# Optimization experiments

Measured on AMD Instinct MI355X. Metric: run time of the kernel, lower is better.

Reference implementation:

```python
import jax, jax.numpy as jnp
import numpy as np

N_OBJ = 4096
IN_DIM = 1024
OUT_DIM = 1024
H = OUT_DIM // 2  # per-direction hidden, BidirectionalTreeLSTM uses out_dim//2
L = 2             # num_layer


def _build_tree(n):
    # balanced binary heap tree: node i has children 2i+1, 2i+2
    left = np.array([2 * i + 1 if 2 * i + 1 < n else -1 for i in range(n)], np.int32)
    right = np.array([2 * i + 2 if 2 * i + 2 < n else -1 for i in range(n)], np.int32)
    parent = np.full(n, -1, np.int32)
    for i in range(n):
        if left[i] >= 0:
            parent[left[i]] = i
        if right[i] >= 0:
            parent[right[i]] = i
    post, stack = [], [(0, False)]
    while stack:
        node, seen = stack.pop()
        if node < 0:
            continue
        if seen:
            post.append(node)
        else:
            stack.append((node, True))
            stack.append((int(right[node]), False))
            stack.append((int(left[node]), False))
    pre, stack = [], [0]
    while stack:
        node = stack.pop()
        if node < 0:
            continue
        pre.append(node)
        stack.append(int(right[node]))
        stack.append(int(left[node]))
    pad = lambda a: np.where(a < 0, n, a).astype(np.int32)  # slot n = zeros (no child/parent)
    return (np.array(post, np.int32), np.array(pre, np.int32),
            pad(left), pad(right), pad(parent))


def setup_inputs() -> dict:
    key = jax.random.key(0)
    ks = jax.random.split(key, 8)
    post, pre, left, right, parent = _build_tree(N_OBJ)

    def w(k, shape, fan_in):
        return jax.random.normal(k, shape, jnp.float32) * np.float32(1.0 / np.sqrt(fan_in))

    # bias init per the torch module: forget-gate blocks get constants, rest zero
    fw_bl = np.zeros((L, 6 * H), np.float32); fw_bl[:, 2 * H:4 * H] = 0.5
    fw_br = fw_bl.copy()
    bw_bh = np.zeros((L, 5 * H), np.float32); bw_bh[:, 2 * H:3 * H] = 1.0

    return {
        "features": jax.random.normal(ks[0], (N_OBJ, IN_DIM), jnp.float32),
        "fw_Wp": w(ks[1], (L, H, IN_DIM), IN_DIM),
        "fw_bp": jnp.zeros((L, H), jnp.float32),
        "fw_Wx": w(ks[2], (L, 6 * H, IN_DIM), IN_DIM),
        "fw_bx": jnp.zeros((L, 6 * H), jnp.float32),
        "fw_Wl": w(ks[3], (L, 6 * H, H), H),
        "fw_bl": jnp.asarray(fw_bl),
        "fw_Wr": w(ks[4], (L, 6 * H, H), H),
        "fw_br": jnp.asarray(fw_br),
        "bw_Wp": w(ks[5], (L, H, IN_DIM), IN_DIM),
        "bw_bp": jnp.zeros((L, H), jnp.float32),
        "bw_Wx": w(ks[6], (L, 5 * H, IN_DIM), IN_DIM),
        "bw_bx": jnp.zeros((L, 5 * H), jnp.float32),
        "bw_Wh": w(ks[7], (L, 5 * H, H), H),
        "bw_bh": jnp.asarray(bw_bh),
        "post_order": jnp.asarray(post),
        "pre_order": jnp.asarray(pre),
        "left_child": jnp.asarray(left),
        "right_child": jnp.asarray(right),
        "parent": jnp.asarray(parent),
    }


def _tree_leaves_to_root(feats, Wp, bp, Wx, bx, Wl, bl, Wr, br,
                         post_order, left_child, right_child):
    n = feats.shape[0]
    h = bp.shape[0]
    px = feats @ Wp.T + bp   # [n, h]   -- self path
    x2 = feats @ Wx.T + bx   # [n, 6h]  -- gate input, batched once

    def step(carry, idx):
        cbuf, hbuf = carry   # [n+1, h]; row n is permanent zero slot for missing children
        lc = left_child[idx]
        rc = right_child[idx]
        g = x2[idx] + hbuf[lc] @ Wl.T + bl + hbuf[rc] @ Wr.T + br
        i, o, fl, fr, u, r = jnp.split(g, 6)
        i = jax.nn.sigmoid(i); o = jax.nn.sigmoid(o)
        fl = jax.nn.sigmoid(fl); fr = jax.nn.sigmoid(fr)
        u = jnp.tanh(u); r = jax.nn.sigmoid(r)
        c = i * u + fl * cbuf[lc] + fr * cbuf[rc]
        hc = o * jnp.tanh(c)
        hf = r * hc + (1.0 - r) * px[idx]   # highway mix
        return (cbuf.at[idx].set(c), hbuf.at[idx].set(hf)), None

    init = (jnp.zeros((n + 1, h), feats.dtype), jnp.zeros((n + 1, h), feats.dtype))
    (_, hbuf), _ = jax.lax.scan(step, init, post_order)
    return hbuf[:n]


def _tree_root_to_leaves(feats, Wp, bp, Wx, bx, Wh, bh, pre_order, parent):
    n = feats.shape[0]
    h = bp.shape[0]
    px = feats @ Wp.T + bp   # [n, h]
    x2 = feats @ Wx.T + bx   # [n, 5h]

    def step(carry, idx):
        cbuf, hbuf = carry
        p = parent[idx]      # root maps to zero slot n -> iofuh(0) == bias, as in torch
        g = x2[idx] + hbuf[p] @ Wh.T + bh
        i, o, f, u, r = jnp.split(g, 5)
        i = jax.nn.sigmoid(i); o = jax.nn.sigmoid(o)
        f = jax.nn.sigmoid(f); u = jnp.tanh(u); r = jax.nn.sigmoid(r)
        c = i * u + f * cbuf[p]
        hc = o * jnp.tanh(c)
        hf = r * hc + (1.0 - r) * px[idx]
        return (cbuf.at[idx].set(c), hbuf.at[idx].set(hf)), None

    init = (jnp.zeros((n + 1, h), feats.dtype), jnp.zeros((n + 1, h), feats.dtype))
    (_, hbuf), _ = jax.lax.scan(step, init, pre_order)
    return hbuf[:n]


def reference(features, fw_Wp, fw_bp, fw_Wx, fw_bx, fw_Wl, fw_bl, fw_Wr, fw_br,
              bw_Wp, bw_bp, bw_Wx, bw_bx, bw_Wh, bw_bh,
              post_order, pre_order, left_child, right_child, parent):
    feats = features
    for l in range(L):  # MultiLayer_BTreeLSTM: stacked bidirectional layers
        h_fwd = _tree_leaves_to_root(feats, fw_Wp[l], fw_bp[l], fw_Wx[l], fw_bx[l],
                                     fw_Wl[l], fw_bl[l], fw_Wr[l], fw_br[l],
                                     post_order, left_child, right_child)
        h_bwd = _tree_root_to_leaves(feats, bw_Wp[l], bw_bp[l], bw_Wx[l], bw_bx[l],
                                     bw_Wh[l], bw_bh[l], pre_order, parent)
        feats = jnp.concatenate([h_fwd, h_bwd], axis=1)  # [n, out_dim]
    return feats
```

## Files before the change

### kernel.cpp

```cpp
#include <hip/hip_runtime.h>
#include <cstdint>
#include <cstddef>


#define HDIM 512
#define ZROW 4096
#define NCAT 6656

typedef _Float16 f16;
typedef f16   f16x8 __attribute__((ext_vector_type(8)));
typedef float f32x4 __attribute__((ext_vector_type(4)));

__device__ __forceinline__ float sigm(float x) { return 1.0f / (1.0f + expf(-x)); }

__device__ __forceinline__ void glds16(const f16* g, f16* l)
{
    __builtin_amdgcn_global_load_lds(
        (const __attribute__((address_space(1))) void*)g,
        (__attribute__((address_space(3))) void*)l,
        16, 0, 0);
}

#define WAIT_VM4()  do { asm volatile("s_waitcnt vmcnt(4)" ::: "memory"); \
                         __builtin_amdgcn_sched_barrier(0); } while (0)
#define WAIT_VM0()  do { asm volatile("s_waitcnt vmcnt(0)" ::: "memory"); \
                         __builtin_amdgcn_sched_barrier(0); } while (0)
#define BARRIER()   do { __builtin_amdgcn_s_barrier(); \
                         __builtin_amdgcn_sched_barrier(0); } while (0)

__device__ __forceinline__ void cvt8s(const float* __restrict__ s, f16* __restrict__ d)
{
    float4 v0 = ((const float4*)s)[0];
    float4 v1 = ((const float4*)s)[1];
    f16x8 o;
    o[0] = (f16)v0.x; o[1] = (f16)v0.y; o[2] = (f16)v0.z; o[3] = (f16)v0.w;
    o[4] = (f16)v1.x; o[5] = (f16)v1.y; o[6] = (f16)v1.z; o[7] = (f16)v1.w;
    *(f16x8*)d = o;
}

__global__ __launch_bounds__(256) void cvt16(
    const float* __restrict__ s, f16* __restrict__ d, int n8)
{
    int i = blockIdx.x * 256 + threadIdx.x;
    if (i >= n8) return;
    cvt8s(s + (size_t)i * 8, d + (size_t)i * 8);
}

__global__ __launch_bounds__(256) void prep_layer(
    const float* __restrict__ fWp, const float* __restrict__ fWx,
    const float* __restrict__ bWp, const float* __restrict__ bWx,
    const float* __restrict__ fWl, const float* __restrict__ fWr,
    const float* __restrict__ bWh,
    const float* __restrict__ fbp, const float* __restrict__ fbx,
    const float* __restrict__ bbp, const float* __restrict__ bbx,
    f16* __restrict__ Wcat, f16* __restrict__ Wlr, f16* __restrict__ Wh,
    float* __restrict__ biascat)
{
    const int bid = blockIdx.x;
    const int t   = threadIdx.x;
    if (bid < 256) {
        int i = bid * 256 + t;
        cvt8s(fWp + (size_t)i * 8, Wcat + (size_t)i * 8);
    } else if (bid < 1792) {
        int i = (bid - 256) * 256 + t;
        cvt8s(fWx + (size_t)i * 8, Wcat + (size_t)512 * 1024 + (size_t)i * 8);
    } else if (bid < 2048) {
        int i = (bid - 1792) * 256 + t;
        cvt8s(bWp + (size_t)i * 8, Wcat + (size_t)3584 * 1024 + (size_t)i * 8);
    } else if (bid < 3328) {
        int i = (bid - 2048) * 256 + t;
        cvt8s(bWx + (size_t)i * 8, Wcat + (size_t)4096 * 1024 + (size_t)i * 8);
    } else if (bid < 4864) {
        int i = (bid - 3328) * 256 + t;
        int col8 = (i * 8) & 1023;
        int row  = (i * 8) >> 10;
        const float* s = (col8 < HDIM) ? (fWl + (size_t)row * HDIM + col8)
                                       : (fWr + (size_t)row * HDIM + col8 - HDIM);
        int np = (row & 511) * 6 + (row >> 9);
        cvt8s(s, Wlr + (size_t)np * 1024 + col8);
    } else if (bid < 5504) {
        int i = (bid - 4864) * 256 + t;
        int col8 = (i * 8) & 511;
        int row  = (i * 8) >> 9;
        int np = (row & 511) * 5 + (row >> 9);
        cvt8s(bWh + (size_t)row * HDIM + col8, Wh + (size_t)np * HDIM + col8);
    } else {
        int i = (bid - 5504) * 256 + t;
        if (i >= NCAT) return;
        float v;
        if (i < 512) v = fbp[i];
        else if (i < 3584) v = fbx[i - 512];
        else if (i < 4096) v = bbp[i - 3584];
        else v = bbx[i - 4096];
        biascat[i] = v;
    }
}

__global__ void zero_slots(f16* H, float* cbf, float* cbb)
{
    int t = threadIdx.x;
    H[(size_t)ZROW * 1024 + t] = (f16)0.0f;
    if (t < HDIM) {
        cbf[(size_t)ZROW * HDIM + t] = 0.0f;
        cbb[(size_t)ZROW * HDIM + t] = 0.0f;
    }
}

__global__ __launch_bounds__(256) void mm_pre(
    const f16* __restrict__ A, const f16* __restrict__ W,
    const float* __restrict__ bias, f16* __restrict__ C, int N, int K)
{
    __shared__ __align__(16) f16 Ab[3][128 * 32];
    __shared__ __align__(16) f16 Bb[3][128 * 32];
    const int t  = threadIdx.x;
    const int L  = t & 63;
    const int w  = t >> 6;
    const int wm = (w & 1) << 6;
    const int wn = (w >> 1) << 6;
    const int fr = L & 15;
    const int fq = L >> 4;
    const int la  = L >> 2;
    const int cs  = (((L & 3) ^ ((L >> 3) & 3)) << 3);

    const f16* a0 = A + (size_t)(blockIdx.y * 128 + w * 16 + la) * K + cs;
    const f16* a1 = a0 + (size_t)64 * K;
    const f16* b0 = W + (size_t)(blockIdx.x * 128 + w * 16 + la) * K + cs;
    const f16* b1 = b0 + (size_t)64 * K;
    const int lo = w * 512 + L * 8;
    const int hi = lo + 2048;

    f32x4 acc[4][4] = {};
    const int nt = K >> 5;
    const int fsw = ((fr >> 1) & 3) << 3;

#define STG_P(sel, k0)                       \
    do {                                     \
        glds16(a0 + (k0), &Ab[sel][lo]);     \
        glds16(a1 + (k0), &Ab[sel][hi]);     \
        glds16(b0 + (k0), &Bb[sel][lo]);     \
        glds16(b1 + (k0), &Bb[sel][hi]);     \
    } while (0)

    STG_P(0, 0);
    STG_P(1, 32);
    int cur = 0, nxt2 = 2;
    for (int tt = 0; tt < nt; ++tt) {
        if (tt + 2 < nt) { WAIT_VM4(); } else { WAIT_VM0(); }
        BARRIER();
        if (tt + 2 < nt) STG_P(nxt2, (tt + 2) << 5);
        f16x8 af[4], bg[4];
#pragma unroll
        for (int i = 0; i < 4; ++i)
            af[i] = *(const f16x8*)(&Ab[cur][(wm + i * 16 + fr) * 32 + ((fq << 3) ^ fsw)]);
#pragma unroll
        for (int j = 0; j < 4; ++j)
            bg[j] = *(const f16x8*)(&Bb[cur][(wn + j * 16 + fr) * 32 + ((fq << 3) ^ fsw)]);
#pragma unroll
        for (int i = 0; i < 4; ++i)
#pragma unroll
            for (int j = 0; j < 4; ++j)
                acc[i][j] = __builtin_amdgcn_mfma_f32_16x16x32_f16(
                    af[i], bg[j], acc[i][j], 0, 0, 0);
        cur = (cur == 2) ? 0 : cur + 1;
        nxt2 = (nxt2 == 2) ? 0 : nxt2 + 1;
    }
#undef STG_P

    const int gr0 = blockIdx.y * 128 + wm + fq * 4;
    const int gc0 = blockIdx.x * 128 + wn + fr;
#pragma unroll
    for (int j = 0; j < 4; ++j) {
        const int gc = gc0 + j * 16;
        const float bj = bias[gc];
#pragma unroll
        for (int i = 0; i < 4; ++i) {
            const int gr = gr0 + i * 16;
#pragma unroll
            for (int rr = 0; rr < 4; ++rr)
                C[(size_t)(gr + rr) * N + gc] = (f16)(acc[i][j][rr] + bj);
        }
    }
}

__global__ __launch_bounds__(256) void stage_fused(
    const f16* __restrict__ Wlr, const f16* __restrict__ Wh,
    f16* H, const f16* __restrict__ PX,
    const int* __restrict__ lc, const int* __restrict__ rc,
    const int* __restrict__ par,
    int fbase, int fm, int bbase, int bm,
    float* __restrict__ cbf, float* __restrict__ cbb,
    float* out32,
    const float* __restrict__ bl, const float* __restrict__ br,
    const float* __restrict__ bh)
{
    __shared__ __align__(16) char smem[57344];
    f16*   Ab0 = (f16*)smem;
    f16*   Bb0 = (f16*)(smem + 32768);
    float* Sg  = (float*)smem;

    const int t   = threadIdx.x;
    const int L   = t & 63;
    const int w   = t >> 6;
    const int fr  = L & 15;
    const int fq  = L >> 4;
    const int rch = L >> 3;
    const int cs  = (((L & 7) ^ rch) << 3);
    const int fsw = (fr & 7) << 3;
    const int nfB = ((fm + 127) >> 7) * 32;

    if ((int)blockIdx.x < nfB) {
        const int by = blockIdx.x >> 5;
        const int bx = blockIdx.x & 31;
        const int wm = (w & 1) << 6;
        const int wn = (w >> 1) * 48;

        const f16* aLo[4]; const f16* aHi[4];
#pragma unroll
        for (int cc = 0; cc < 4; ++cc) {
            int g  = by * 128 + (w * 4 + cc) * 8 + rch;
            int n1 = ZROW, n2 = ZROW;
            if (g < fm) { n1 = lc[fbase + g]; n2 = rc[fbase + g]; }
            aLo[cc] = H + (size_t)n1 * 1024 + cs;
            aHi[cc] = H + (size_t)n2 * 1024 + cs - HDIM;
        }
        const f16* bsrc[3];
#pragma unroll
        for (int cc = 0; cc < 3; ++cc)
            bsrc[cc] = Wlr + (size_t)(bx * 96 + (w * 3 + cc) * 8 + rch) * 1024 + cs;

        f32x4 acc[4][3] = {};
#define STGF(sel, k0)                                                        \
        do {                                                                 \
            const bool hiK = (k0) >= HDIM;                                   \
            _Pragma("unroll")                                                \
            for (int cc = 0; cc < 4; ++cc)                                   \
                glds16((hiK ? aHi[cc] : aLo[cc]) + (k0),                     \
                       Ab0 + (sel) * 8192 + (w * 4 + cc) * 512 + L * 8);     \
            _Pragma("unroll")                                                \
            for (int cc = 0; cc < 3; ++cc)                                   \
                glds16(bsrc[cc] + (k0),                                      \
                       Bb0 + (sel) * 6144 + (w * 3 + cc) * 512 + L * 8);     \
        } while (0)

        STGF(0, 0);
        __syncthreads();
        int cur = 0;
        for (int tt = 0; tt < 16; ++tt) {
            if (tt + 1 < 16) STGF(cur ^ 1, (tt + 1) * 64);
            const f16* Ac = Ab0 + cur * 8192;
            const f16* Bc = Bb0 + cur * 6144;
            f16x8 af[4][2], bg[3][2];
#pragma unroll
            for (int i = 0; i < 4; ++i)
#pragma unroll
                for (int ks = 0; ks < 2; ++ks)
                    af[i][ks] = *(const f16x8*)(Ac + (wm + i * 16 + fr) * 64
                                + ((((ks * 4 + fq) << 3) ^ fsw)));
#pragma unroll
            for (int j = 0; j < 3; ++j)
#pragma unroll
                for (int ks = 0; ks < 2; ++ks)
                    bg[j][ks] = *(const f16x8*)(Bc + (wn + j * 16 + fr) * 64
                                + ((((ks * 4 + fq) << 3) ^ fsw)));
#pragma unroll
            for (int ks = 0; ks < 2; ++ks)
#pragma unroll
                for (int i = 0; i < 4; ++i)
#pragma unroll
                    for (int j = 0; j < 3; ++j)
                        acc[i][j] = __builtin_amdgcn_mfma_f32_16x16x32_f16(
                            af[i][ks], bg[j][ks], acc[i][j], 0, 0, 0);
            __syncthreads();
            cur ^= 1;
        }
#undef STGF
#pragma unroll
        for (int i = 0; i < 4; ++i)
#pragma unroll
            for (int j = 0; j < 3; ++j)
#pragma unroll
                for (int rr = 0; rr < 4; ++rr)
                    Sg[(wm + i * 16 + fq * 4 + rr) * 100 + wn + j * 16 + fr]
                        = acc[i][j][rr];
        __syncthreads();
        const int rmax = fm - by * 128;
        const int j0 = bx * 16;
        for (int cc = 0; cc < 8; ++cc) {
            int cell = t + cc * 256;
            int r = cell >> 4, j = cell & 15;
            if (r >= rmax) break;
            int node = fbase + by * 128 + r;
            int jj = j0 + j;
            const f16* pxr = PX + (size_t)node * NCAT;
            float g[6];
#pragma unroll
            for (int q = 0; q < 6; ++q)
                g[q] = (float)pxr[HDIM + q * HDIM + jj] + bl[q * HDIM + jj]
                     + br[q * HDIM + jj] + Sg[r * 100 + j * 6 + q];
            int lcn = lc[node], rcn = rc[node];
            float clv = cbf[(size_t)lcn * HDIM + jj];
            float crv = cbf[(size_t)rcn * HDIM + jj];
            float i_ = sigm(g[0]), o_ = sigm(g[1]), fl_ = sigm(g[2]), fr_ = sigm(g[3]);
            float u_ = tanhf(g[4]), r_ = sigm(g[5]);
            float c  = i_ * u_ + fl_ * clv + fr_ * crv;
            float hc = o_ * tanhf(c);
            float px = (float)pxr[jj];
            float hf = r_ * hc + (1.0f - r_) * px;
            cbf[(size_t)node * HDIM + jj] = c;
            H[(size_t)node * 1024 + jj] = (f16)hf;
            if (out32) out32[(size_t)node * 1024 + jj] = hf;
        }
    } else {
        const int b2 = blockIdx.x - nfB;
        const int by = b2 >> 5;
        const int bx = b2 & 31;
        const int wm = w * 32;

        const f16* asrc[4];
#pragma unroll
        for (int cc = 0; cc < 4; ++cc) {
            int g = by * 128 + (w * 4 + cc) * 8 + rch;
            int n1 = ZROW;
            if (g < bm) n1 = par[bbase + g];
            asrc[cc] = H + (size_t)n1 * 1024 + HDIM + cs;
        }
        const f16* bsrc[3];
        int nbch[3];
#pragma unroll
        for (int cc = 0; cc < 3; ++cc) {
            int ch = w * 3 + cc;
            nbch[cc] = ch;
            bsrc[cc] = Wh + (size_t)(bx * 80 + ch * 8 + rch) * HDIM + cs;
        }

        f32x4 acc[2][5] = {};
#define STGB(sel, k0)                                                        \
        do {                                                                 \
            _Pragma("unroll")                                                \
            for (int cc = 0; cc < 4; ++cc)                                   \
                glds16(asrc[cc] + (k0),                                      \
                       Ab0 + (sel) * 8192 + (w * 4 + cc) * 512 + L * 8);     \
            _Pragma("unroll")                                                \
            for (int cc = 0; cc < 3; ++cc)                                   \
                if (nbch[cc] < 10)                                           \
                    glds16(bsrc[cc] + (k0),                                  \
                           Bb0 + (sel) * 5120 + nbch[cc] * 512 + L * 8);     \
        } while (0)

        STGB(0, 0);
        __syncthreads();
        int cur = 0;
        for (int tt = 0; tt < 8; ++tt) {
            if (tt + 1 < 8) STGB(cur ^ 1, (tt + 1) * 64);
            const f16* Ac = Ab0 + cur * 8192;
            const f16* Bc = Bb0 + cur * 5120;
            f16x8 af[2][2], bg[5][2];
#pragma unroll
            for (int i = 0; i < 2; ++i)
#pragma unroll
                for (int ks = 0; ks < 2; ++ks)
                    af[i][ks] = *(const f16x8*)(Ac + (wm + i * 16 + fr) * 64
                                + ((((ks * 4 + fq) << 3) ^ fsw)));
#pragma unroll
            for (int j = 0; j < 5; ++j)
#pragma unroll
                for (int ks = 0; ks < 2; ++ks)
                    bg[j][ks] = *(const f16x8*)(Bc + ((j) * 16 + fr) * 64
                                + ((((ks * 4 + fq) << 3) ^ fsw)));
#pragma unroll
            for (int ks = 0; ks < 2; ++ks)
#pragma unroll
                for (int i = 0; i < 2; ++i)
#pragma unroll
                    for (int j = 0; j < 5; ++j)
                        acc[i][j] = __builtin_amdgcn_mfma_f32_16x16x32_f16(
                            af[i][ks], bg[j][ks], acc[i][j], 0, 0, 0);
            __syncthreads();
            cur ^= 1;
        }
#undef STGB
#pragma unroll
        for (int i = 0; i < 2; ++i)
#pragma unroll
            for (int j = 0; j < 5; ++j)
#pragma unroll
                for (int rr = 0; rr < 4; ++rr)
                    Sg[(wm + i * 16 + fq * 4 + rr) * 84 + j * 16 + fr]
                        = acc[i][j][rr];
        __syncthreads();
        const int rmax = bm - by * 128;
        const int j0 = bx * 16;
        for (int cc = 0; cc < 8; ++cc) {
            int cell = t + cc * 256;
            int r = cell >> 4, j = cell & 15;
            if (r >= rmax) break;
            int node = bbase + by * 128 + r;
            int jj = j0 + j;
            const f16* pxr = PX + (size_t)node * NCAT;
            float g[5];
#pragma unroll
            for (int q = 0; q < 5; ++q)
                g[q] = (float)pxr[4096 + q * HDIM + jj] + bh[q * HDIM + jj]
                     + Sg[r * 84 + j * 5 + q];
            int p = par[node];
            float cp = cbb[(size_t)p * HDIM + jj];
            float i_ = sigm(g[0]), o_ = sigm(g[1]), f_ = sigm(g[2]);
            float u_ = tanhf(g[3]), r_ = sigm(g[4]);
            float c  = i_ * u_ + f_ * cp;
            float hc = o_ * tanhf(c);
            float px = (float)pxr[3584 + jj];
            float hf = r_ * hc + (1.0f - r_) * px;
            cbb[(size_t)node * HDIM + jj] = c;
            H[(size_t)node * 1024 + HDIM + jj] = (f16)hf;
            if (out32) out32[(size_t)node * 1024 + HDIM + jj] = hf;
        }
    }
}

__global__ __launch_bounds__(256) void elem_merged(
    const f16* __restrict__ PX,
    int fbase, int fm, int bbase, int bm,
    const int* __restrict__ lc, const int* __restrict__ rc,
    const int* __restrict__ par,
    float* __restrict__ cbf, float* __restrict__ cbb,
    f16* __restrict__ H, float* __restrict__ out32,
    const float* __restrict__ bl, const float* __restrict__ br,
    const float* __restrict__ bh)
{
    int t = blockIdx.x * 256 + threadIdx.x;
    const int fvec = fm * 64;
    if (t < fvec) {
        int row = t >> 6, j8 = (t & 63) << 3;
        int node = fbase + row;
        const f16* pxr = PX + (size_t)node * NCAT;
        float g[6][8];
#pragma unroll
        for (int q = 0; q < 6; ++q) {
            f16x8 pv = *(const f16x8*)(pxr + HDIM + q * HDIM + j8);
            const float* blp = bl + q * HDIM + j8;
            const float* brp = br + q * HDIM + j8;
#pragma unroll
            for (int e = 0; e < 8; ++e)
                g[q][e] = (float)pv[e] + blp[e] + brp[e];
        }
        int lcn = lc[node], rcn = rc[node];
        const float* clp = cbf + (size_t)lcn * HDIM + j8;
        const float* crp = cbf + (size_t)rcn * HDIM + j8;
        f32x4 cl0 = *(const f32x4*)clp, cl1 = *(const f32x4*)(clp + 4);
        f32x4 cr0 = *(const f32x4*)crp, cr1 = *(const f32x4*)(crp + 4);
        f16x8 pxv = *(const f16x8*)(pxr + j8);
        f32x4 co0, co1;
        f16x8 hv;
        f32x4 ho0, ho1;
#pragma unroll
        for (int e = 0; e < 8; ++e) {
            float clv = (e < 4) ? cl0[e & 3] : cl1[e & 3];
            float crv = (e < 4) ? cr0[e & 3] : cr1[e & 3];
            float i_ = sigm(g[0][e]), o_ = sigm(g[1][e]);
            float fl_ = sigm(g[2][e]), fr_ = sigm(g[3][e]);
            float u_ = tanhf(g[4][e]), r_ = sigm(g[5][e]);
            float c  = i_ * u_ + fl_ * clv + fr_ * crv;
            float hc = o_ * tanhf(c);
            float hf = r_ * hc + (1.0f - r_) * (float)pxv[e];
            if (e < 4) { co0[e & 3] = c; ho0[e & 3] = hf; }
            else       { co1[e & 3] = c; ho1[e & 3] = hf; }
            hv[e] = (f16)hf;
        }
        float* cdst = cbf + (size_t)node * HDIM + j8;
        *(f32x4*)cdst = co0; *(f32x4*)(cdst + 4) = co1;
        *(f16x8*)(H + (size_t)node * 1024 + j8) = hv;
        if (out32) {
            float* od = out32 + (size_t)node * 1024 + j8;
            *(f32x4*)od = ho0; *(f32x4*)(od + 4) = ho1;
        }
    } else {
        int t2 = t - fvec;
        if (t2 >= bm * 64) return;
        int row = t2 >> 6, j8 = (t2 & 63) << 3;
        int node = bbase + row;
        const f16* pxr = PX + (size_t)node * NCAT;
        float g[5][8];
#pragma unroll
        for (int q = 0; q < 5; ++q) {
            f16x8 pv = *(const f16x8*)(pxr + 4096 + q * HDIM + j8);
            const float* bhp = bh + q * HDIM + j8;
#pragma unroll
            for (int e = 0; e < 8; ++e)
                g[q][e] = (float)pv[e] + bhp[e];
        }
        int p = par[node];
        const float* cpp = cbb + (size_t)p * HDIM + j8;
        f32x4 cp0 = *(const f32x4*)cpp, cp1 = *(const f32x4*)(cpp + 4);
        f16x8 pxv = *(const f16x8*)(pxr + 3584 + j8);
        f32x4 co0, co1;
        f16x8 hv;
        f32x4 ho0, ho1;
#pragma unroll
        for (int e = 0; e < 8; ++e) {
            float cpv = (e < 4) ? cp0[e & 3] : cp1[e & 3];
            float i_ = sigm(g[0][e]), o_ = sigm(g[1][e]), f_ = sigm(g[2][e]);
            float u_ = tanhf(g[3][e]), r_ = sigm(g[4][e]);
            float c  = i_ * u_ + f_ * cpv;
            float hc = o_ * tanhf(c);
            float hf = r_ * hc + (1.0f - r_) * (float)pxv[e];
            if (e < 4) { co0[e & 3] = c; ho0[e & 3] = hf; }
            else       { co1[e & 3] = c; ho1[e & 3] = hf; }
            hv[e] = (f16)hf;
        }
        float* cdst = cbb + (size_t)node * HDIM + j8;
        *(f32x4*)cdst = co0; *(f32x4*)(cdst + 4) = co1;
        *(f16x8*)(H + (size_t)node * 1024 + HDIM + j8) = hv;
        if (out32) {
            float* od = out32 + (size_t)node * 1024 + HDIM + j8;
            *(f32x4*)od = ho0; *(f32x4*)(od + 4) = ho1;
        }
    }
}

extern "C" void kernel_launch(void* const* d_in, const int* in_sizes, int n_in,
                              void* d_out, int out_size, void* d_ws, size_t ws_size,
                              hipStream_t stream)
{
    (void)in_sizes; (void)n_in; (void)out_size; (void)ws_size;
    const float* features = (const float*)d_in[0];
    const float* fw_Wp = (const float*)d_in[1];
    const float* fw_bp = (const float*)d_in[2];
    const float* fw_Wx = (const float*)d_in[3];
    const float* fw_bx = (const float*)d_in[4];
    const float* fw_Wl = (const float*)d_in[5];
    const float* fw_bl = (const float*)d_in[6];
    const float* fw_Wr = (const float*)d_in[7];
    const float* fw_br = (const float*)d_in[8];
    const float* bw_Wp = (const float*)d_in[9];
    const float* bw_bp = (const float*)d_in[10];
    const float* bw_Wx = (const float*)d_in[11];
    const float* bw_bx = (const float*)d_in[12];
    const float* bw_Wh = (const float*)d_in[13];
    const float* bw_bh = (const float*)d_in[14];
    const int* lc  = (const int*)d_in[17];
    const int* rc  = (const int*)d_in[18];
    const int* par = (const int*)d_in[19];

    f16* feat16 = (f16*)d_ws;
    f16* H      = feat16 + (size_t)4096 * 1024;
    f16* Wcat   = H     + (size_t)4097 * 1024;
    f16* Wlr    = Wcat  + (size_t)NCAT * 1024;
    f16* Wh     = Wlr   + (size_t)3072 * 1024;
    f16* PX     = Wh    + (size_t)2560 * 512;
    float* biascat = (float*)(PX + (size_t)4096 * NCAT);
    float* cbf     = biascat + NCAT;
    float* cbb     = cbf + (size_t)4097 * HDIM;

    zero_slots<<<dim3(1), dim3(1024), 0, stream>>>(H, cbf, cbb);
    cvt16<<<dim3(2048), 256, 0, stream>>>(features, feat16, 4096 * 1024 / 8);

    static const int fb[12] = {2047, 1023, 511, 255, 127, 63, 31, 15, 7, 3, 1, 0};
    static const int fmv[12] = {1, 1024, 512, 256, 128, 64, 32, 16, 8, 4, 2, 1};
    static const int bb[12] = {1, 3, 7, 15, 31, 63, 127, 255, 511, 1023, 2047, 4095};
    static const int bmv[12] = {2, 4, 8, 16, 32, 64, 128, 256, 512, 1024, 2048, 1};

    for (int l = 0; l < 2; ++l) {
        prep_layer<<<dim3(5530), 256, 0, stream>>>(
            fw_Wp + (size_t)l * 512 * 1024,  fw_Wx + (size_t)l * 3072 * 1024,
            bw_Wp + (size_t)l * 512 * 1024,  bw_Wx + (size_t)l * 2560 * 1024,
            fw_Wl + (size_t)l * 3072 * 512,  fw_Wr + (size_t)l * 3072 * 512,
            bw_Wh + (size_t)l * 2560 * 512,
            fw_bp + (size_t)l * 512, fw_bx + (size_t)l * 3072,
            bw_bp + (size_t)l * 512, bw_bx + (size_t)l * 2560,
            Wcat, Wlr, Wh, biascat);

        const f16* A16 = (l == 0) ? feat16 : H;
        mm_pre<<<dim3(NCAT / 128, 4096 / 128), 256, 0, stream>>>(
            A16, Wcat, biascat, PX, NCAT, 1024);

        float* o32 = (l == 1) ? (float*)d_out : nullptr;
        const float* bl_l = fw_bl + (size_t)l * 3072;
        const float* br_l = fw_br + (size_t)l * 3072;
        const float* bh_l = bw_bh + (size_t)l * 2560;

        {
            int tot = (2048 + 1) * 64;
            elem_merged<<<dim3((tot + 255) / 256), 256, 0, stream>>>(
                PX, 2048, 2048, 0, 1,
                lc, rc, par, cbf, cbb, H, o32, bl_l, br_l, bh_l);
        }
        for (int i = 0; i < 12; ++i) {
            int nfB = ((fmv[i] + 127) >> 7) * 32;
            int nbB = ((bmv[i] + 127) >> 7) * 32;
            stage_fused<<<dim3(nfB + nbB), 256, 0, stream>>>(
                Wlr, Wh, H, PX, lc, rc, par,
                fb[i], fmv[i], bb[i], bmv[i],
                cbf, cbb, o32, bl_l, br_l, bh_l);
        }
    }
}
```

Measured before the change: 795.1 us.

## Rewrite input-projection GEMM as 256x256 tile, 8-wave kernel with split-phase pipelining

Replaces the 128x128, 4-wave, triple-buffered projection GEMM with a 256x256 tile, 8-wave kernel. It uses a K-step of 64, double-buffered LDS, and an XOR swizzle. Each iteration is split into four quarter phases that interleave global-to-LDS prefetches, barriers and MFMA blocks, with s_setprio raised around the MFMA clusters. The aim is more data reuse per loaded tile and better overlap of memory and matrix work. The cost is 128KB of LDS per block, higher register pressure, and fewer blocks (26x16) to fill the GPU.

Result: faster. 776.6 us (-2.3%).

```diff
diff --git a/kernel.cpp b/kernel.cpp
--- a/kernel.cpp
+++ b/kernel.cpp
@@ -21,12 +21,14 @@
         16, 0, 0);
 }
 
-#define WAIT_VM4()  do { asm volatile("s_waitcnt vmcnt(4)" ::: "memory"); \
-                         __builtin_amdgcn_sched_barrier(0); } while (0)
-#define WAIT_VM0()  do { asm volatile("s_waitcnt vmcnt(0)" ::: "memory"); \
-                         __builtin_amdgcn_sched_barrier(0); } while (0)
+#define WAIT_VM6()  asm volatile("s_waitcnt vmcnt(6)" ::: "memory")
+#define WAIT_VM4()  asm volatile("s_waitcnt vmcnt(4)" ::: "memory")
+#define WAIT_VM2()  asm volatile("s_waitcnt vmcnt(2)" ::: "memory")
+#define WAIT_VM0()  asm volatile("s_waitcnt vmcnt(0)" ::: "memory")
 #define BARRIER()   do { __builtin_amdgcn_s_barrier(); \
                          __builtin_amdgcn_sched_barrier(0); } while (0)
+#define SP1()       __builtin_amdgcn_s_setprio(1)
+#define SP0()       __builtin_amdgcn_s_setprio(0)
 
 __device__ __forceinline__ void cvt8s(const float* __restrict__ s, f16* __restrict__ d)
 {
@@ -106,74 +108,108 @@
     }
 }
 
-__global__ __launch_bounds__(256) void mm_pre(
+__global__ __launch_bounds__(512) void mm_pre8(
     const f16* __restrict__ A, const f16* __restrict__ W,
     const float* __restrict__ bias, f16* __restrict__ C, int N, int K)
 {
-    __shared__ __align__(16) f16 Ab[3][128 * 32];
-    __shared__ __align__(16) f16 Bb[3][128 * 32];
-    const int t  = threadIdx.x;
-    const int L  = t & 63;
-    const int w  = t >> 6;
-    const int wm = (w & 1) << 6;
-    const int wn = (w >> 1) << 6;
-    const int fr = L & 15;
-    const int fq = L >> 4;
-    const int la  = L >> 2;
-    const int cs  = (((L & 3) ^ ((L >> 3) & 3)) << 3);
-
-    const f16* a0 = A + (size_t)(blockIdx.y * 128 + w * 16 + la) * K + cs;
-    const f16* a1 = a0 + (size_t)64 * K;
-    const f16* b0 = W + (size_t)(blockIdx.x * 128 + w * 16 + la) * K + cs;
-    const f16* b1 = b0 + (size_t)64 * K;
-    const int lo = w * 512 + L * 8;
-    const int hi = lo + 2048;
-
-    f32x4 acc[4][4] = {};
-    const int nt = K >> 5;
-    const int fsw = ((fr >> 1) & 3) << 3;
-
-#define STG_P(sel, k0)                       \
-    do {                                     \
-        glds16(a0 + (k0), &Ab[sel][lo]);     \
-        glds16(a1 + (k0), &Ab[sel][hi]);     \
-        glds16(b0 + (k0), &Bb[sel][lo]);     \
-        glds16(b1 + (k0), &Bb[sel][hi]);     \
+    __shared__ __align__(16) f16 lds[2][2][16384];
+    const int t   = threadIdx.x;
+    const int L   = t & 63;
+    const int wid = t >> 6;
+    const int wr  = wid >> 2;
+    const int wc  = wid & 3;
+    const int fr  = L & 15;
+    const int fq  = L >> 4;
+    const int srow = t >> 3;
+    const int cs   = (((t & 7) ^ (srow & 7)) << 3);
+    const int vrow = ((srow >> 5) << 6) + (srow & 31);
+    const int bB0  = (srow >= 32) ? 2048 : 0;
+    const f16* Ag = A + (size_t)(blockIdx.y * 256) * K + cs;
+    const f16* Bg = W + (size_t)(blockIdx.x * 256) * K + cs;
+    const int xa0 = ((fq)     ^ (fr & 7)) << 3;
+    const int xa1 = ((4 + fq) ^ (fr & 7)) << 3;
+
+#define STG_A(nb, T, u)                                                      \
+    do {                                                                     \
+        glds16(Ag + (size_t)(srow + (u) * 64) * K + (T) * 64,                \
+               &lds[nb][0][(u) * 4096 + t * 8]);                             \
+        glds16(Ag + (size_t)(srow + (u) * 64 + 128) * K + (T) * 64,          \
+               &lds[nb][0][(u) * 4096 + 8192 + t * 8]);                      \
     } while (0)
-
-    STG_P(0, 0);
-    STG_P(1, 32);
-    int cur = 0, nxt2 = 2;
-    for (int tt = 0; tt < nt; ++tt) {
-        if (tt + 2 < nt) { WAIT_VM4(); } else { WAIT_VM0(); }
+#define STG_B(nb, T, v)                                                      \
+    do {                                                                     \
+        glds16(Bg + (size_t)(vrow + (v) * 32) * K + (T) * 64,                \
+               &lds[nb][1][(v) * 2048 + bB0 + t * 8]);                       \
+        glds16(Bg + (size_t)(vrow + (v) * 32 + 128) * K + (T) * 64,          \
+               &lds[nb][1][(v) * 2048 + bB0 + 8192 + t * 8]);                \
+    } while (0)
+
+    f32x4 acc[8][4] = {};
+    f16x8 afr[4][2], bf0[2][2], bf1[2][2];
+
+#define LDA(Ar, mh)                                                          \
+    do {                                                                     \
+        _Pragma("unroll") for (int i2 = 0; i2 < 4; ++i2) {                   \
+            afr[i2][0] = *(const f16x8*)((Ar) + ((mh) * 64 + i2 * 16) * 64 + xa0); \
+            afr[i2][1] = *(const f16x8*)((Ar) + ((mh) * 64 + i2 * 16) * 64 + xa1); \
+        }                                                                    \
+    } while (0)
+#define LDB(Br, BF, nh)                                                      \
+    do {                                                                     \
+        _Pragma("unroll") for (int j2 = 0; j2 < 2; ++j2) {                   \
+            BF[j2][0] = *(const f16x8*)((Br) + ((nh) * 32 + j2 * 16) * 64 + xa0); \
+            BF[j2][1] = *(const f16x8*)((Br) + ((nh) * 32 + j2 * 16) * 64 + xa1); \
+        }                                                                    \
+    } while (0)
+#define MF(mh, nh, BF)                                                       \
+    do {                                                                     \
+        _Pragma("unroll") for (int ks = 0; ks < 2; ++ks)                     \
+        _Pragma("unroll") for (int i2 = 0; i2 < 4; ++i2)                     \
+        _Pragma("unroll") for (int j2 = 0; j2 < 2; ++j2)                     \
+            acc[(mh) * 4 + i2][(nh) * 2 + j2] =                              \
+                __builtin_amdgcn_mfma_f32_16x16x32_f16(                      \
+                    afr[i2][ks], BF[j2][ks],                                 \
+                    acc[(mh) * 4 + i2][(nh) * 2 + j2], 0, 0, 0);             \
+    } while (0)
+
+    const int NT = K >> 6;
+    STG_A(0, 0, 0); STG_B(0, 0, 0); STG_B(0, 0, 1); STG_A(0, 0, 1);
+
+    for (int T = 0; T < NT; ++T) {
+        const int cb = T & 1, nb = cb ^ 1;
+        const bool pf = (T + 1 < NT);
+        const f16* Ar = &lds[cb][0][(wr * 128 + fr) * 64];
+        const f16* Br = &lds[cb][1][(wc * 64 + fr) * 64];
+        if (pf) { STG_A(nb, T + 1, 0); WAIT_VM6(); } else { WAIT_VM4(); }
         BARRIER();
-        if (tt + 2 < nt) STG_P(nxt2, (tt + 2) << 5);
-        f16x8 af[4], bg[4];
-#pragma unroll
-        for (int i = 0; i < 4; ++i)
-            af[i] = *(const f16x8*)(&Ab[cur][(wm + i * 16 + fr) * 32 + ((fq << 3) ^ fsw)]);
-#pragma unroll
-        for (int j = 0; j < 4; ++j)
-            bg[j] = *(const f16x8*)(&Bb[cur][(wn + j * 16 + fr) * 32 + ((fq << 3) ^ fsw)]);
-#pragma unroll
-        for (int i = 0; i < 4; ++i)
-#pragma unroll
-            for (int j = 0; j < 4; ++j)
-                acc[i][j] = __builtin_amdgcn_mfma_f32_16x16x32_f16(
-                    af[i], bg[j], acc[i][j], 0, 0, 0);
-        cur = (cur == 2) ? 0 : cur + 1;
-        nxt2 = (nxt2 == 2) ? 0 : nxt2 + 1;
+        LDA(Ar, 0); LDB(Br, bf0, 0);
+        SP1(); MF(0, 0, bf0); SP0();
+        if (pf) { STG_B(nb, T + 1, 0); WAIT_VM6(); } else { WAIT_VM2(); }
+        BARRIER();
+        LDB(Br, bf1, 1);
+        SP1(); MF(0, 1, bf1); SP0();
+        if (pf) { STG_B(nb, T + 1, 1); WAIT_VM6(); } else { WAIT_VM0(); }
+        BARRIER();
+        LDA(Ar, 1);
+        SP1(); MF(1, 1, bf1); SP0();
+        if (pf) STG_A(nb, T + 1, 1);
+        BARRIER();
+        SP1(); MF(1, 0, bf0); SP0();
     }
-#undef STG_P
-
-    const int gr0 = blockIdx.y * 128 + wm + fq * 4;
-    const int gc0 = blockIdx.x * 128 + wn + fr;
+#undef STG_A
+#undef STG_B
+#undef LDA
+#undef LDB
+#undef MF
+
+    const int gr0 = blockIdx.y * 256 + wr * 128 + fq * 4;
+    const int gc0 = blockIdx.x * 256 + wc * 64 + fr;
 #pragma unroll
     for (int j = 0; j < 4; ++j) {
         const int gc = gc0 + j * 16;
         const float bj = bias[gc];
 #pragma unroll
-        for (int i = 0; i < 4; ++i) {
+        for (int i = 0; i < 8; ++i) {
             const int gr = gr0 + i * 16;
 #pragma unroll
             for (int rr = 0; rr < 4; ++rr)
@@ -570,7 +606,7 @@
             Wcat, Wlr, Wh, biascat);
 
         const f16* A16 = (l == 0) ? feat16 : H;
-        mm_pre<<<dim3(NCAT / 128, 4096 / 128), 256, 0, stream>>>(
+        mm_pre8<<<dim3(NCAT / 256, 4096 / 256), 512, 0, stream>>>(
             A16, Wcat, biascat, PX, NCAT, 1024);
 
         float* o32 = (l == 1) ? (float*)d_out : nullptr;
```
